# Kernel tuning notes

Hardware: AMD Instinct MI355X
Metric: run time of the kernel (lower is better)

## Reference

```python
import jax, jax.numpy as jnp
import numpy as np

P = 8          # patch_size
HEADS = 4      # patch_size // 2
DIM = 256      # nf*P*P // 16
DH = DIM // HEADS


def setup_inputs() -> dict:
    key = jax.random.key(0)
    ks = jax.random.split(key, 8)
    B, N, C, H, W = 8, 1, 64, 256, 256
    Np = (H // P) * (W // P)           # 1024
    patch_dim = C * P * P              # 4096
    s = 0.02
    return {
        "x": jax.random.normal(ks[0], (B, N, C, H, W), jnp.float32),
        "W_embed": jax.random.normal(ks[1], (DIM, patch_dim), jnp.float32) * s,
        "b_embed": jnp.zeros((DIM,), jnp.float32),
        "pos": jax.random.normal(ks[2], (1, Np, DIM), jnp.float32),
        "Wq": jax.random.normal(ks[3], (DIM, DIM), jnp.float32) * s,
        "Wk": jax.random.normal(ks[4], (Np, Np), jnp.float32) * s,
        "Wv": jax.random.normal(ks[5], (DIM, DIM), jnp.float32) * s,
        "Wout": jax.random.normal(ks[6], (patch_dim, DIM), jnp.float32) * s,
        "b_out": jnp.zeros((patch_dim,), jnp.float32),
    }


def reference(x, W_embed, b_embed, pos, Wq, Wk, Wv, Wout, b_out):
    B, N, C, H, W = x.shape
    Hp, Wp = H // P, W // P
    Np = Hp * Wp
    patch_dim = C * P * P
    BN = B * N

    # unfold (non-overlapping patches), column order = (C, kh, kw)
    xb = x.reshape(BN, C, Hp, P, Wp, P)
    patches = xb.transpose(0, 2, 4, 1, 3, 5).reshape(BN, Np, patch_dim)

    # linear_embed + positional embedding
    emb = jnp.einsum('bnp,dp->bnd', patches, W_embed) + b_embed + pos  # (BN, Np, DIM)

    # q: linear, split heads, mean over head-dim (AvgPool1d(dh) on length dh)
    q = jnp.einsum('bnd,ed->bne', emb, Wq)
    q = q.reshape(BN, Np, HEADS, DH).transpose(0, 2, 1, 3)  # (BN, H, Np, DH)
    q = q.mean(axis=-1)                                      # (BN, H, Np)

    # k = sigmoid(linear_k(q)); diag_embed(k) @ v == k[..., None] * v
    k = jax.nn.sigmoid(jnp.einsum('bhn,mn->bhm', q, Wk))     # (BN, H, Np)

    v = jnp.einsum('bnd,ed->bne', emb, Wv)
    v = v.reshape(BN, Np, HEADS, DH).transpose(0, 2, 1, 3)   # (BN, H, Np, DH)

    out = k[..., None] * v                                   # (BN, H, Np, DH)
    out = out.transpose(0, 2, 1, 3).reshape(BN, Np, DIM)

    out = jnp.einsum('bnd,pd->bnp', out, Wout) + b_out       # (BN, Np, patch_dim)

    # fold back to image
    out = out.reshape(BN, Hp, Wp, C, P, P).transpose(0, 3, 1, 4, 2, 5)
    out = out.reshape(B, N, C, H, W)
    return out
```

## Files before the change

### kernel.cpp

```cpp
#include <hip/hip_runtime.h>

typedef __attribute__((ext_vector_type(8))) short short8;
typedef __attribute__((ext_vector_type(4))) float f32x4;

#define LDA 72
#define KST 260

__device__ __forceinline__ unsigned short f2bf(float f) {
  unsigned int u = __builtin_bit_cast(unsigned int, f);
  u += 0x7fffu + ((u >> 16) & 1u);
  return (unsigned short)(u >> 16);
}
__device__ __forceinline__ float bf2f(unsigned short us) {
  return __builtin_bit_cast(float, (unsigned int)us << 16);
}

__device__ __forceinline__ void cvt_block(const float* __restrict__ src,
                                          unsigned short* __restrict__ dst, int b) {
  int i = b * 256 + threadIdx.x;
  float4 f = ((const float4*)src)[i];
  unsigned int lo = (unsigned int)f2bf(f.x) | ((unsigned int)f2bf(f.y) << 16);
  unsigned int hi = (unsigned int)f2bf(f.z) | ((unsigned int)f2bf(f.w) << 16);
  uint2 u; u.x = lo; u.y = hi;
  ((uint2*)dst)[i] = u;
}

__global__ __launch_bounds__(256) void prep_kernel(
    const float* __restrict__ W_embed, const float* __restrict__ Wout,
    const float* __restrict__ Wv, const float* __restrict__ Wq,
    unsigned short* __restrict__ Wb, unsigned short* __restrict__ Wob,
    unsigned short* __restrict__ Wvb, float* __restrict__ WqR) {
  int b = blockIdx.x;
  if (b < 1024) { cvt_block(W_embed, Wb, b); return; }
  if (b < 2048) { cvt_block(Wout, Wob, b - 1024); return; }
  if (b < 2112) { cvt_block(Wv, Wvb, b - 2048); return; }
  int idx = (b - 2112) * 256 + threadIdx.x;
  int h = idx >> 8, e = idx & 255;
  float s = 0.f;
  for (int j = 0; j < 64; ++j) s += Wq[(size_t)(h * 64 + j) * 256 + e];
  WqR[idx] = s * (1.f / 64.f);
}

__global__ __launch_bounds__(256) void gemm1_embed(
    const float* __restrict__ x, const unsigned short* __restrict__ Wb,
    float* __restrict__ part) {
  __shared__ __align__(16) unsigned short As[64 * LDA];
  __shared__ __align__(16) unsigned short Bs[128 * LDA];
  const int nt = blockIdx.x, mt = blockIdx.y, sk = blockIdx.z;
  const int m0 = mt * 64, n0 = nt * 128;
  const int t = threadIdx.x;
  const int wave = t >> 6, lane = t & 63;
  const int wm = wave >> 1, wn = wave & 1;
  const int lr = lane & 15, lq = lane >> 4;
  f32x4 acc[2][4];
#pragma unroll
  for (int i = 0; i < 2; i++)
#pragma unroll
    for (int j = 0; j < 4; j++) acc[i][j] = f32x4{0.f, 0.f, 0.f, 0.f};

  for (int kt = sk * 16; kt < sk * 16 + 16; ++kt) {
    const int k0 = kt * 64;
#pragma unroll
    for (int rr = 0; rr < 2; ++rr) {
      int r = t + rr * 256;
      int m = r >> 3, krun = r & 7;
      int gm = m0 + m;
      int bn = gm >> 10, nn = gm & 1023;
      int ph = nn >> 5, pw = nn & 31;
      int k = k0 + krun * 8;
      int c = k >> 6, kh = (k >> 3) & 7;
      const float* src = x + ((size_t)((bn << 6) + c) << 16) +
                         (size_t)((ph << 3) + kh) * 256 + (pw << 3);
      float4 f0 = *(const float4*)src;
      float4 f1 = *(const float4*)(src + 4);
      short8 v;
      v[0] = (short)f2bf(f0.x); v[1] = (short)f2bf(f0.y);
      v[2] = (short)f2bf(f0.z); v[3] = (short)f2bf(f0.w);
      v[4] = (short)f2bf(f1.x); v[5] = (short)f2bf(f1.y);
      v[6] = (short)f2bf(f1.z); v[7] = (short)f2bf(f1.w);
      *(short8*)&As[m * LDA + krun * 8] = v;
    }
#pragma unroll
    for (int rr = 0; rr < 4; ++rr) {
      int r = t + rr * 256;
      int n = r >> 3, krun = r & 7;
      *(short8*)&Bs[n * LDA + krun * 8] =
          *(const short8*)(Wb + (size_t)(n0 + n) * 4096 + k0 + krun * 8);
    }
    __syncthreads();
#pragma unroll
    for (int kc = 0; kc < 2; ++kc) {
      short8 a0 = *(const short8*)&As[(wm * 32 + lr) * LDA + kc * 32 + lq * 8];
      short8 a1 = *(const short8*)&As[(wm * 32 + 16 + lr) * LDA + kc * 32 + lq * 8];
#pragma unroll
      for (int ni = 0; ni < 4; ++ni) {
        short8 b = *(const short8*)&Bs[(wn * 64 + ni * 16 + lr) * LDA + kc * 32 + lq * 8];
        acc[0][ni] = __builtin_amdgcn_mfma_f32_16x16x32_bf16(a0, b, acc[0][ni], 0, 0, 0);
        acc[1][ni] = __builtin_amdgcn_mfma_f32_16x16x32_bf16(a1, b, acc[1][ni], 0, 0, 0);
      }
    }
    __syncthreads();
  }
  float* pdst = part + (size_t)sk * 2097152;
#pragma unroll
  for (int mi = 0; mi < 2; ++mi)
#pragma unroll
    for (int ni = 0; ni < 4; ++ni) {
      int col = n0 + wn * 64 + ni * 16 + lr;
      int rbase = m0 + wm * 32 + mi * 16 + lq * 4;
#pragma unroll
      for (int r2 = 0; r2 < 4; ++r2)
        pdst[(size_t)(rbase + r2) * 256 + col] = acc[mi][ni][r2];
    }
}

__global__ __launch_bounds__(256) void finq_kernel(
    const float* __restrict__ part, const float* __restrict__ b_embed,
    const float* __restrict__ pos, const float* __restrict__ WqR,
    unsigned short* __restrict__ emb_bf, float* __restrict__ q) {
  __shared__ float wq[1024];
  const int t = threadIdx.x;
  for (int i = t; i < 1024; i += 256) wq[i] = WqR[i];
  __syncthreads();
  const int row_l = t >> 3, seg = t & 7;
  const int row = blockIdx.x * 32 + row_l;
  const int bn = row >> 10, n = row & 1023;
  const float4* p4 = (const float4*)part;
  const float4* b4 = (const float4*)b_embed;
  const float4* pos4 = (const float4*)pos;
  const float4* wq4 = (const float4*)wq;
  const int idx0 = row * 64 + seg * 8;

  float4 e[8];
#pragma unroll
  for (int j = 0; j < 8; ++j) {
    float4 v = p4[idx0 + j];
    float4 v1 = p4[524288 + idx0 + j];
    float4 v2 = p4[1048576 + idx0 + j];
    float4 v3 = p4[1572864 + idx0 + j];
    float4 bb = b4[seg * 8 + j];
    float4 pp = pos4[(size_t)n * 64 + seg * 8 + j];
    e[j].x = v.x + v1.x + v2.x + v3.x + bb.x + pp.x;
    e[j].y = v.y + v1.y + v2.y + v3.y + bb.y + pp.y;
    e[j].z = v.z + v1.z + v2.z + v3.z + bb.z + pp.z;
    e[j].w = v.w + v1.w + v2.w + v3.w + bb.w + pp.w;
  }
  unsigned int ub[16];
#pragma unroll
  for (int j = 0; j < 8; ++j) {
    ub[2 * j]     = (unsigned int)f2bf(e[j].x) | ((unsigned int)f2bf(e[j].y) << 16);
    ub[2 * j + 1] = (unsigned int)f2bf(e[j].z) | ((unsigned int)f2bf(e[j].w) << 16);
  }
  uint4* dst = (uint4*)(emb_bf + (size_t)row * 256 + seg * 32);
#pragma unroll
  for (int j = 0; j < 4; ++j)
    dst[j] = make_uint4(ub[4 * j], ub[4 * j + 1], ub[4 * j + 2], ub[4 * j + 3]);
  float s[4] = {0.f, 0.f, 0.f, 0.f};
#pragma unroll
  for (int h = 0; h < 4; ++h)
#pragma unroll
    for (int j = 0; j < 8; ++j) {
      float4 w = wq4[h * 64 + seg * 8 + j];
      s[h] += e[j].x * w.x + e[j].y * w.y + e[j].z * w.z + e[j].w * w.w;
    }
#pragma unroll
  for (int h = 0; h < 4; ++h) {
    s[h] += __shfl_xor(s[h], 1);
    s[h] += __shfl_xor(s[h], 2);
    s[h] += __shfl_xor(s[h], 4);
  }
  if (seg == 0) {
#pragma unroll
    for (int h = 0; h < 4; ++h)
      q[(size_t)(bn * 4 + h) * 1024 + n] = s[h];
  }
}

__global__ __launch_bounds__(256) void k_kernel(const float* __restrict__ q,
                                                const float* __restrict__ Wk,
                                                float* __restrict__ kk) {
  __shared__ float wk_s[8 * KST];
  __shared__ float q_s[32 * KST];
  const int m0 = blockIdx.x * 8;
  const int t = threadIdx.x;
  const int m = t & 7, bh = t >> 3;
  const float4* wkg = (const float4*)Wk;
  const float4* qg = (const float4*)q;
  float acc = 0.f;
  for (int kt = 0; kt < 4; ++kt) {
    const int k0 = kt * 256;
#pragma unroll
    for (int i = 0; i < 2; ++i) {
      int idx = t + i * 256;
      int r = idx >> 6, c4 = idx & 63;
      *(float4*)&wk_s[r * KST + c4 * 4] = wkg[((size_t)(m0 + r) * 1024 + k0) / 4 + c4];
    }
#pragma unroll
    for (int i = 0; i < 8; ++i) {
      int idx = t + i * 256;
      int r = idx >> 6, c4 = idx & 63;
      *(float4*)&q_s[r * KST + c4 * 4] = qg[((size_t)r * 1024 + k0) / 4 + c4];
    }
    __syncthreads();
#pragma unroll 8
    for (int k4 = 0; k4 < 64; ++k4) {
      float4 a = *(const float4*)&wk_s[m * KST + k4 * 4];
      float4 b = *(const float4*)&q_s[bh * KST + k4 * 4];
      acc += a.x * b.x + a.y * b.y + a.z * b.z + a.w * b.w;
    }
    __syncthreads();
  }
  kk[(size_t)bh * 1024 + m0 + m] = 1.f / (1.f + __expf(-acc));
}

__global__ __launch_bounds__(256) void vgemm_kernel(
    const unsigned short* __restrict__ Abf, const unsigned short* __restrict__ Wvb,
    const float* __restrict__ kk, unsigned short* __restrict__ ov) {
  __shared__ __align__(16) unsigned short As[32 * LDA];
  __shared__ __align__(16) unsigned short Bs[64 * LDA];
  const int nt = blockIdx.x, mt = blockIdx.y;
  const int m0 = mt * 32, n0 = nt * 64;
  const int t = threadIdx.x;
  const int wave = t >> 6, lane = t & 63;
  const int wr = wave >> 1, wc = wave & 1;
  const int lr = lane & 15, lq = lane >> 4;
  f32x4 acc[2];
  acc[0] = f32x4{0.f, 0.f, 0.f, 0.f};
  acc[1] = f32x4{0.f, 0.f, 0.f, 0.f};

  for (int kt = 0; kt < 4; ++kt) {
    const int k0 = kt * 64;
    {
      int m = t >> 3, krun = t & 7;
      *(short8*)&As[m * LDA + krun * 8] =
          *(const short8*)(Abf + (size_t)(m0 + m) * 256 + k0 + krun * 8);
    }
#pragma unroll
    for (int rr = 0; rr < 2; ++rr) {
      int r = t + rr * 256;
      int n = r >> 3, krun = r & 7;
      *(short8*)&Bs[n * LDA + krun * 8] =
          *(const short8*)(Wvb + (size_t)(n0 + n) * 256 + k0 + krun * 8);
    }
    __syncthreads();
#pragma unroll
    for (int kc = 0; kc < 2; ++kc) {
      short8 a = *(const short8*)&As[(wr * 16 + lr) * LDA + kc * 32 + lq * 8];
#pragma unroll
      for (int ni = 0; ni < 2; ++ni) {
        short8 b = *(const short8*)&Bs[(wc * 32 + ni * 16 + lr) * LDA + kc * 32 + lq * 8];
        acc[ni] = __builtin_amdgcn_mfma_f32_16x16x32_bf16(a, b, acc[ni], 0, 0, 0);
      }
    }
    __syncthreads();
  }
#pragma unroll
  for (int ni = 0; ni < 2; ++ni) {
    int col = n0 + wc * 32 + ni * 16 + lr;
    int h = col >> 6;
    int rbase = m0 + wr * 16 + lq * 4;
#pragma unroll
    for (int r2 = 0; r2 < 4; ++r2) {
      int row = rbase + r2;
      int bn = row >> 10, n = row & 1023;
      float g = kk[(size_t)(bn * 4 + h) * 1024 + n];
      ov[(size_t)row * 256 + col] = f2bf(acc[ni][r2] * g);
    }
  }
}

#define CST 132
__global__ __launch_bounds__(256) void gemm2_out(
    const unsigned short* __restrict__ Abf, const unsigned short* __restrict__ Wob,
    const float* __restrict__ b_out, float* __restrict__ out) {
  __shared__ __align__(16) float smem[64 * CST];
  unsigned short* As = (unsigned short*)smem;
  unsigned short* Bs = As + 64 * LDA;
  const int nt = blockIdx.x, mt = blockIdx.y;
  const int m0 = mt * 64, n0 = nt * 128;
  const int t = threadIdx.x;
  const int wave = t >> 6, lane = t & 63;
  const int wm = wave >> 1, wn = wave & 1;
  const int lr = lane & 15, lq = lane >> 4;
  f32x4 acc[2][4];
#pragma unroll
  for (int i = 0; i < 2; i++)
#pragma unroll
    for (int j = 0; j < 4; j++) acc[i][j] = f32x4{0.f, 0.f, 0.f, 0.f};

  for (int kt = 0; kt < 4; ++kt) {
    const int k0 = kt * 64;
#pragma unroll
    for (int rr = 0; rr < 2; ++rr) {
      int r = t + rr * 256;
      int m = r >> 3, krun = r & 7;
      *(short8*)&As[m * LDA + krun * 8] =
          *(const short8*)(Abf + (size_t)(m0 + m) * 256 + k0 + krun * 8);
    }
#pragma unroll
    for (int rr = 0; rr < 4; ++rr) {
      int r = t + rr * 256;
      int n = r >> 3, krun = r & 7;
      *(short8*)&Bs[n * LDA + krun * 8] =
          *(const short8*)(Wob + (size_t)(n0 + n) * 256 + k0 + krun * 8);
    }
    __syncthreads();
#pragma unroll
    for (int kc = 0; kc < 2; ++kc) {
      short8 a0 = *(const short8*)&As[(wm * 32 + lr) * LDA + kc * 32 + lq * 8];
      short8 a1 = *(const short8*)&As[(wm * 32 + 16 + lr) * LDA + kc * 32 + lq * 8];
#pragma unroll
      for (int ni = 0; ni < 4; ++ni) {
        short8 b = *(const short8*)&Bs[(wn * 64 + ni * 16 + lr) * LDA + kc * 32 + lq * 8];
        acc[0][ni] = __builtin_amdgcn_mfma_f32_16x16x32_bf16(a0, b, acc[0][ni], 0, 0, 0);
        acc[1][ni] = __builtin_amdgcn_mfma_f32_16x16x32_bf16(a1, b, acc[1][ni], 0, 0, 0);
      }
    }
    __syncthreads();
  }
#pragma unroll
  for (int mi = 0; mi < 2; ++mi)
#pragma unroll
    for (int ni = 0; ni < 4; ++ni) {
      int pl = wn * 64 + ni * 16 + lr;
      int mb = wm * 32 + mi * 16 + lq * 4;
#pragma unroll
      for (int r2 = 0; r2 < 4; ++r2)
        smem[(mb + r2) * CST + pl] = acc[mi][ni][r2];
    }
  __syncthreads();
  const int bn = m0 >> 10;
  const int ph0 = (m0 & 1023) >> 5;
  const int c0 = n0 >> 6;
#pragma unroll
  for (int i = 0; i < 8; ++i) {
    int idx4 = t + i * 256;
    int kw4 = idx4 & 1;
    int pw = (idx4 >> 1) & 31;
    int kh = (idx4 >> 6) & 7;
    int c2 = (idx4 >> 9) & 1;
    int ph = (idx4 >> 10) & 1;
    int m_local = ph * 32 + pw;
    int p_local = c2 * 64 + kh * 8 + kw4 * 4;
    float4 v = *(const float4*)&smem[m_local * CST + p_local];
    float4 bo = *(const float4*)(b_out + n0 + p_local);
    v.x += bo.x; v.y += bo.y; v.z += bo.z; v.w += bo.w;
    size_t addr = ((size_t)((bn << 6) + c0 + c2) << 16) +
                  (size_t)(((ph0 + ph) << 3) + kh) * 256 + (pw << 3) + kw4 * 4;
    *(float4*)(out + addr) = v;
  }
}

extern "C" void kernel_launch(void* const* d_in, const int* in_sizes, int n_in,
                              void* d_out, int out_size, void* d_ws, size_t ws_size,
                              hipStream_t stream) {
  const float* x       = (const float*)d_in[0];
  const float* W_embed = (const float*)d_in[1];
  const float* b_embed = (const float*)d_in[2];
  const float* pos     = (const float*)d_in[3];
  const float* Wq      = (const float*)d_in[4];
  const float* Wk      = (const float*)d_in[5];
  const float* Wv      = (const float*)d_in[6];
  const float* Wout    = (const float*)d_in[7];
  const float* b_out   = (const float*)d_in[8];
  float* out = (float*)d_out;

  char* ws = (char*)d_ws;
  const size_t MB = 1024 * 1024;
  float* part            = (float*)(ws);
  unsigned short* ov     = (unsigned short*)(ws);
  unsigned short* emb_bf = (unsigned short*)(ws + 32 * MB);
  unsigned short* Wb     = (unsigned short*)(ws + 36 * MB);
  unsigned short* Wob    = (unsigned short*)(ws + 38 * MB);
  unsigned short* Wvb    = (unsigned short*)(ws + 40 * MB);
  float* q               = (float*)(ws + 40 * MB + 131072);
  float* kk              = (float*)(ws + 40 * MB + 262144);
  float* WqR             = (float*)(ws + 40 * MB + 393216);

  prep_kernel<<<2116, 256, 0, stream>>>(W_embed, Wout, Wv, Wq, Wb, Wob, Wvb, WqR);
  gemm1_embed<<<dim3(2, 128, 4), 256, 0, stream>>>(x, Wb, part);
  finq_kernel<<<256, 256, 0, stream>>>(part, b_embed, pos, WqR, emb_bf, q);
  k_kernel<<<128, 256, 0, stream>>>(q, Wk, kk);
  vgemm_kernel<<<dim3(4, 256), 256, 0, stream>>>(emb_bf, Wvb, kk, ov);
  gemm2_out<<<dim3(32, 128), 256, 0, stream>>>(ov, Wob, b_out, out);
}
```

Baseline: 357.1 us.

## Double-buffer gemm1 shared tiles with register prefetch and coalesced patch loads

The embedding GEMM now uses 512-thread blocks with 128x128 tiles and double-buffered LDS. The next k-tile is prefetched into registers while MFMAs run on the current buffer, which leaves one barrier per iteration instead of two. The A-tile loads are reorganised so a warp reads contiguous image rows of a patch row, giving more coalesced global loads. The trade-off is more LDS per block and higher register pressure, which may limit occupancy.

```diff
diff --git a/kernel.cpp b/kernel.cpp
--- a/kernel.cpp
+++ b/kernel.cpp
@@ -41,66 +41,114 @@
   WqR[idx] = s * (1.f / 64.f);
 }
 
-__global__ __launch_bounds__(256) void gemm1_embed(
+__global__ __launch_bounds__(512, 4) void gemm1_embed(
     const float* __restrict__ x, const unsigned short* __restrict__ Wb,
     float* __restrict__ part) {
-  __shared__ __align__(16) unsigned short As[64 * LDA];
-  __shared__ __align__(16) unsigned short Bs[128 * LDA];
+  __shared__ __align__(16) unsigned short sm[2][2][128 * LDA];
   const int nt = blockIdx.x, mt = blockIdx.y, sk = blockIdx.z;
-  const int m0 = mt * 64, n0 = nt * 128;
+  const int m0 = mt * 128, n0 = nt * 128;
   const int t = threadIdx.x;
   const int wave = t >> 6, lane = t & 63;
   const int wm = wave >> 1, wn = wave & 1;
   const int lr = lane & 15, lq = lane >> 4;
+
+  const int bn = m0 >> 10;
+  const int ph0 = (m0 & 1023) >> 5;
+
+  const int uA0 = t >> 5, colA = t & 31;
+  const int uA1 = uA0 + 16;
+  const float* xA = x + ((size_t)(bn << 6) << 16);
+  const float* pa0 = xA + (size_t)(((ph0 + (uA0 >> 3)) << 3) + (uA0 & 7)) * 256 + (colA << 3);
+  const float* pa1 = xA + (size_t)(((ph0 + (uA1 >> 3)) << 3) + (uA1 & 7)) * 256 + (colA << 3);
+  const int dA0 = (((uA0 >> 3) << 5) + colA) * LDA + ((uA0 & 7) << 3);
+  const int dA1 = (((uA1 >> 3) << 5) + colA) * LDA + ((uA1 & 7) << 3);
+
+  const int nB0 = t >> 3, kB = t & 7;
+  const int nB1 = nB0 + 64;
+  const unsigned short* pb0 = Wb + (size_t)(n0 + nB0) * 4096 + (kB << 3);
+  const unsigned short* pb1 = Wb + (size_t)(n0 + nB1) * 4096 + (kB << 3);
+  const int dB0 = nB0 * LDA + (kB << 3);
+  const int dB1 = nB1 * LDA + (kB << 3);
+
   f32x4 acc[2][4];
 #pragma unroll
   for (int i = 0; i < 2; i++)
 #pragma unroll
     for (int j = 0; j < 4; j++) acc[i][j] = f32x4{0.f, 0.f, 0.f, 0.f};
 
-  for (int kt = sk * 16; kt < sk * 16 + 16; ++kt) {
-    const int k0 = kt * 64;
-#pragma unroll
-    for (int rr = 0; rr < 2; ++rr) {
-      int r = t + rr * 256;
-      int m = r >> 3, krun = r & 7;
-      int gm = m0 + m;
-      int bn = gm >> 10, nn = gm & 1023;
-      int ph = nn >> 5, pw = nn & 31;
-      int k = k0 + krun * 8;
-      int c = k >> 6, kh = (k >> 3) & 7;
-      const float* src = x + ((size_t)((bn << 6) + c) << 16) +
-                         (size_t)((ph << 3) + kh) * 256 + (pw << 3);
-      float4 f0 = *(const float4*)src;
-      float4 f1 = *(const float4*)(src + 4);
-      short8 v;
-      v[0] = (short)f2bf(f0.x); v[1] = (short)f2bf(f0.y);
-      v[2] = (short)f2bf(f0.z); v[3] = (short)f2bf(f0.w);
-      v[4] = (short)f2bf(f1.x); v[5] = (short)f2bf(f1.y);
-      v[6] = (short)f2bf(f1.z); v[7] = (short)f2bf(f1.w);
-      *(short8*)&As[m * LDA + krun * 8] = v;
-    }
-#pragma unroll
-    for (int rr = 0; rr < 4; ++rr) {
-      int r = t + rr * 256;
-      int n = r >> 3, krun = r & 7;
-      *(short8*)&Bs[n * LDA + krun * 8] =
-          *(const short8*)(Wb + (size_t)(n0 + n) * 4096 + k0 + krun * 8);
-    }
-    __syncthreads();
+  float4 ra0, ra1, ra2, ra3;
+  short8 rb0, rb1;
+  const int kt0 = sk * 16;
+
+  {
+    const float* q0 = pa0 + (size_t)kt0 * 65536;
+    const float* q1 = pa1 + (size_t)kt0 * 65536;
+    ra0 = *(const float4*)q0; ra1 = *(const float4*)(q0 + 4);
+    ra2 = *(const float4*)q1; ra3 = *(const float4*)(q1 + 4);
+    rb0 = *(const short8*)(pb0 + kt0 * 64);
+    rb1 = *(const short8*)(pb1 + kt0 * 64);
+  }
+  {
+    short8 v0, v1;
+    v0[0] = (short)f2bf(ra0.x); v0[1] = (short)f2bf(ra0.y);
+    v0[2] = (short)f2bf(ra0.z); v0[3] = (short)f2bf(ra0.w);
+    v0[4] = (short)f2bf(ra1.x); v0[5] = (short)f2bf(ra1.y);
+    v0[6] = (short)f2bf(ra1.z); v0[7] = (short)f2bf(ra1.w);
+    v1[0] = (short)f2bf(ra2.x); v1[1] = (short)f2bf(ra2.y);
+    v1[2] = (short)f2bf(ra2.z); v1[3] = (short)f2bf(ra2.w);
+    v1[4] = (short)f2bf(ra3.x); v1[5] = (short)f2bf(ra3.y);
+    v1[6] = (short)f2bf(ra3.z); v1[7] = (short)f2bf(ra3.w);
+    *(short8*)&sm[0][0][dA0] = v0;
+    *(short8*)&sm[0][0][dA1] = v1;
+    *(short8*)&sm[0][1][dB0] = rb0;
+    *(short8*)&sm[0][1][dB1] = rb1;
+  }
+  __syncthreads();
+
+#pragma unroll 2
+  for (int i = 0; i < 16; ++i) {
+    if (i < 15) {
+      const int kt = kt0 + i + 1;
+      const float* q0 = pa0 + (size_t)kt * 65536;
+      const float* q1 = pa1 + (size_t)kt * 65536;
+      ra0 = *(const float4*)q0; ra1 = *(const float4*)(q0 + 4);
+      ra2 = *(const float4*)q1; ra3 = *(const float4*)(q1 + 4);
+      rb0 = *(const short8*)(pb0 + kt * 64);
+      rb1 = *(const short8*)(pb1 + kt * 64);
+    }
+    const unsigned short* Ab = sm[i & 1][0];
+    const unsigned short* Bb = sm[i & 1][1];
 #pragma unroll
     for (int kc = 0; kc < 2; ++kc) {
-      short8 a0 = *(const short8*)&As[(wm * 32 + lr) * LDA + kc * 32 + lq * 8];
-      short8 a1 = *(const short8*)&As[(wm * 32 + 16 + lr) * LDA + kc * 32 + lq * 8];
+      short8 a0 = *(const short8*)&Ab[(wm * 32 + lr) * LDA + kc * 32 + lq * 8];
+      short8 a1 = *(const short8*)&Ab[(wm * 32 + 16 + lr) * LDA + kc * 32 + lq * 8];
 #pragma unroll
       for (int ni = 0; ni < 4; ++ni) {
-        short8 b = *(const short8*)&Bs[(wn * 64 + ni * 16 + lr) * LDA + kc * 32 + lq * 8];
+        short8 b = *(const short8*)&Bb[(wn * 64 + ni * 16 + lr) * LDA + kc * 32 + lq * 8];
         acc[0][ni] = __builtin_amdgcn_mfma_f32_16x16x32_bf16(a0, b, acc[0][ni], 0, 0, 0);
         acc[1][ni] = __builtin_amdgcn_mfma_f32_16x16x32_bf16(a1, b, acc[1][ni], 0, 0, 0);
       }
     }
-    __syncthreads();
-  }
+    if (i < 15) {
+      unsigned short* Aw = sm[(i + 1) & 1][0];
+      unsigned short* Bw = sm[(i + 1) & 1][1];
+      short8 v0, v1;
+      v0[0] = (short)f2bf(ra0.x); v0[1] = (short)f2bf(ra0.y);
+      v0[2] = (short)f2bf(ra0.z); v0[3] = (short)f2bf(ra0.w);
+      v0[4] = (short)f2bf(ra1.x); v0[5] = (short)f2bf(ra1.y);
+      v0[6] = (short)f2bf(ra1.z); v0[7] = (short)f2bf(ra1.w);
+      v1[0] = (short)f2bf(ra2.x); v1[1] = (short)f2bf(ra2.y);
+      v1[2] = (short)f2bf(ra2.z); v1[3] = (short)f2bf(ra2.w);
+      v1[4] = (short)f2bf(ra3.x); v1[5] = (short)f2bf(ra3.y);
+      v1[6] = (short)f2bf(ra3.z); v1[7] = (short)f2bf(ra3.w);
+      *(short8*)&Aw[dA0] = v0;
+      *(short8*)&Aw[dA1] = v1;
+      *(short8*)&Bw[dB0] = rb0;
+      *(short8*)&Bw[dB1] = rb1;
+      __syncthreads();
+    }
+  }
+
   float* pdst = part + (size_t)sk * 2097152;
 #pragma unroll
   for (int mi = 0; mi < 2; ++mi)
@@ -378,7 +426,7 @@
   float* WqR             = (float*)(ws + 40 * MB + 393216);
 
   prep_kernel<<<2116, 256, 0, stream>>>(W_embed, Wout, Wv, Wq, Wb, Wob, Wvb, WqR);
-  gemm1_embed<<<dim3(2, 128, 4), 256, 0, stream>>>(x, Wb, part);
+  gemm1_embed<<<dim3(2, 64, 4), 512, 0, stream>>>(x, Wb, part);
   finq_kernel<<<256, 256, 0, stream>>>(part, b_embed, pos, WqR, emb_bf, q);
   k_kernel<<<128, 256, 0, stream>>>(q, Wk, kk);
   vgemm_kernel<<<dim3(4, 256), 256, 0, stream>>>(emb_bf, Wvb, kk, ov);
```

New measurement: 331.8 us. 1.08x faster.

## Double-buffer GEMM tiles with register prefetch and enlarge embed/v tiles

Applied to the files above, without the earlier changes.

The embed GEMM now uses 512-thread blocks over 128-row tiles, with a patch-aware coalesced load mapping. Its K loop is a two-stage register prefetch into double-buffered shared memory, so global loads overlap the MFMA work. The output GEMM gets the same double-buffered prefetch pipeline. The V GEMM loads its whole K=256 slab into shared memory once, using 64-row tiles, which removes the per-step barriers. These changes raise shared memory and register use per block, which may reduce occupancy.

```diff
diff --git a/kernel.cpp b/kernel.cpp
--- a/kernel.cpp
+++ b/kernel.cpp
@@ -13,6 +13,32 @@
 }
 __device__ __forceinline__ float bf2f(unsigned short us) {
   return __builtin_bit_cast(float, (unsigned int)us << 16);
+}
+
+__device__ __forceinline__ short8 cvt8(float4 lo, float4 hi) {
+  short8 v;
+  v[0] = (short)f2bf(lo.x); v[1] = (short)f2bf(lo.y);
+  v[2] = (short)f2bf(lo.z); v[3] = (short)f2bf(lo.w);
+  v[4] = (short)f2bf(hi.x); v[5] = (short)f2bf(hi.y);
+  v[6] = (short)f2bf(hi.z); v[7] = (short)f2bf(hi.w);
+  return v;
+}
+
+__device__ __forceinline__ void mfma_tile(const unsigned short* __restrict__ Ab,
+                                          const unsigned short* __restrict__ Bb,
+                                          int wm, int wn, int lr, int lq,
+                                          f32x4 (&acc)[2][4]) {
+#pragma unroll
+  for (int kc = 0; kc < 2; ++kc) {
+    short8 a0 = *(const short8*)&Ab[(wm * 32 + lr) * LDA + kc * 32 + lq * 8];
+    short8 a1 = *(const short8*)&Ab[(wm * 32 + 16 + lr) * LDA + kc * 32 + lq * 8];
+#pragma unroll
+    for (int ni = 0; ni < 4; ++ni) {
+      short8 b = *(const short8*)&Bb[(wn * 64 + ni * 16 + lr) * LDA + kc * 32 + lq * 8];
+      acc[0][ni] = __builtin_amdgcn_mfma_f32_16x16x32_bf16(a0, b, acc[0][ni], 0, 0, 0);
+      acc[1][ni] = __builtin_amdgcn_mfma_f32_16x16x32_bf16(a1, b, acc[1][ni], 0, 0, 0);
+    }
+  }
 }
 
 __device__ __forceinline__ void cvt_block(const float* __restrict__ src,
@@ -41,66 +67,90 @@
   WqR[idx] = s * (1.f / 64.f);
 }
 
-__global__ __launch_bounds__(256) void gemm1_embed(
+struct StageG1 { float4 a0, a1, a2, a3; short8 b0, b1; };
+
+__device__ __forceinline__ void g1_load(StageG1& s, const float* q0, const float* q1,
+                                        const unsigned short* b0, const unsigned short* b1) {
+  s.a0 = *(const float4*)q0; s.a1 = *(const float4*)(q0 + 4);
+  s.a2 = *(const float4*)q1; s.a3 = *(const float4*)(q1 + 4);
+  s.b0 = *(const short8*)b0; s.b1 = *(const short8*)b1;
+}
+
+__device__ __forceinline__ void g1_write(unsigned short* Aw, unsigned short* Bw,
+                                         int dA0, int dA1, int dB0, int dB1,
+                                         const StageG1& s) {
+  *(short8*)&Aw[dA0] = cvt8(s.a0, s.a1);
+  *(short8*)&Aw[dA1] = cvt8(s.a2, s.a3);
+  *(short8*)&Bw[dB0] = s.b0;
+  *(short8*)&Bw[dB1] = s.b1;
+}
+
+__global__ __launch_bounds__(512, 4) void gemm1_embed(
     const float* __restrict__ x, const unsigned short* __restrict__ Wb,
     float* __restrict__ part) {
-  __shared__ __align__(16) unsigned short As[64 * LDA];
-  __shared__ __align__(16) unsigned short Bs[128 * LDA];
+  __shared__ __align__(16) unsigned short sm[2][2][128 * LDA];
   const int nt = blockIdx.x, mt = blockIdx.y, sk = blockIdx.z;
-  const int m0 = mt * 64, n0 = nt * 128;
+  const int m0 = mt * 128, n0 = nt * 128;
   const int t = threadIdx.x;
   const int wave = t >> 6, lane = t & 63;
   const int wm = wave >> 1, wn = wave & 1;
   const int lr = lane & 15, lq = lane >> 4;
+
+  const int bn = m0 >> 10;
+  const int ph0 = (m0 & 1023) >> 5;
+
+  const int uA0 = t >> 5, colA = t & 31;
+  const int uA1 = uA0 + 16;
+  const float* xA = x + ((size_t)(bn << 6) << 16);
+  const float* pa0 = xA + (size_t)(((ph0 + (uA0 >> 3)) << 3) + (uA0 & 7)) * 256 + (colA << 3);
+  const float* pa1 = xA + (size_t)(((ph0 + (uA1 >> 3)) << 3) + (uA1 & 7)) * 256 + (colA << 3);
+  const int dA0 = (((uA0 >> 3) << 5) + colA) * LDA + ((uA0 & 7) << 3);
+  const int dA1 = (((uA1 >> 3) << 5) + colA) * LDA + ((uA1 & 7) << 3);
+
+  const int nB0 = t >> 3, kB = t & 7;
+  const int nB1 = nB0 + 64;
+  const unsigned short* pb0 = Wb + (size_t)(n0 + nB0) * 4096 + (kB << 3);
+  const unsigned short* pb1 = Wb + (size_t)(n0 + nB1) * 4096 + (kB << 3);
+  const int dB0 = nB0 * LDA + (kB << 3);
+  const int dB1 = nB1 * LDA + (kB << 3);
+
   f32x4 acc[2][4];
 #pragma unroll
   for (int i = 0; i < 2; i++)
 #pragma unroll
     for (int j = 0; j < 4; j++) acc[i][j] = f32x4{0.f, 0.f, 0.f, 0.f};
 
-  for (int kt = sk * 16; kt < sk * 16 + 16; ++kt) {
-    const int k0 = kt * 64;
-#pragma unroll
-    for (int rr = 0; rr < 2; ++rr) {
-      int r = t + rr * 256;
-      int m = r >> 3, krun = r & 7;
-      int gm = m0 + m;
-      int bn = gm >> 10, nn = gm & 1023;
-      int ph = nn >> 5, pw = nn & 31;
-      int k = k0 + krun * 8;
-      int c = k >> 6, kh = (k >> 3) & 7;
-      const float* src = x + ((size_t)((bn << 6) + c) << 16) +
-                         (size_t)((ph << 3) + kh) * 256 + (pw << 3);
-      float4 f0 = *(const float4*)src;
-      float4 f1 = *(const float4*)(src + 4);
-      short8 v;
-      v[0] = (short)f2bf(f0.x); v[1] = (short)f2bf(f0.y);
-      v[2] = (short)f2bf(f0.z); v[3] = (short)f2bf(f0.w);
-      v[4] = (short)f2bf(f1.x); v[5] = (short)f2bf(f1.y);
-      v[6] = (short)f2bf(f1.z); v[7] = (short)f2bf(f1.w);
-      *(short8*)&As[m * LDA + krun * 8] = v;
-    }
-#pragma unroll
-    for (int rr = 0; rr < 4; ++rr) {
-      int r = t + rr * 256;
-      int n = r >> 3, krun = r & 7;
-      *(short8*)&Bs[n * LDA + krun * 8] =
-          *(const short8*)(Wb + (size_t)(n0 + n) * 4096 + k0 + krun * 8);
-    }
+  unsigned short* A0 = &sm[0][0][0]; unsigned short* B0 = &sm[0][1][0];
+  unsigned short* A1 = &sm[1][0][0]; unsigned short* B1 = &sm[1][1][0];
+
+  StageG1 st0, st1;
+  const int kt0 = sk * 16;
+  g1_load(st0, pa0 + (size_t)kt0 * 65536, pa1 + (size_t)kt0 * 65536,
+          pb0 + (size_t)kt0 * 64, pb1 + (size_t)kt0 * 64);
+  g1_load(st1, pa0 + (size_t)(kt0 + 1) * 65536, pa1 + (size_t)(kt0 + 1) * 65536,
+          pb0 + (size_t)(kt0 + 1) * 64, pb1 + (size_t)(kt0 + 1) * 64);
+  g1_write(A0, B0, dA0, dA1, dB0, dB1, st0);
+  __syncthreads();
+
+#pragma unroll 1
+  for (int p = 0; p < 7; ++p) {
+    const int kb = kt0 + 2 * p;
+    g1_load(st0, pa0 + (size_t)(kb + 2) * 65536, pa1 + (size_t)(kb + 2) * 65536,
+            pb0 + (size_t)(kb + 2) * 64, pb1 + (size_t)(kb + 2) * 64);
+    mfma_tile(A0, B0, wm, wn, lr, lq, acc);
+    g1_write(A1, B1, dA0, dA1, dB0, dB1, st1);
     __syncthreads();
-#pragma unroll
-    for (int kc = 0; kc < 2; ++kc) {
-      short8 a0 = *(const short8*)&As[(wm * 32 + lr) * LDA + kc * 32 + lq * 8];
-      short8 a1 = *(const short8*)&As[(wm * 32 + 16 + lr) * LDA + kc * 32 + lq * 8];
-#pragma unroll
-      for (int ni = 0; ni < 4; ++ni) {
-        short8 b = *(const short8*)&Bs[(wn * 64 + ni * 16 + lr) * LDA + kc * 32 + lq * 8];
-        acc[0][ni] = __builtin_amdgcn_mfma_f32_16x16x32_bf16(a0, b, acc[0][ni], 0, 0, 0);
-        acc[1][ni] = __builtin_amdgcn_mfma_f32_16x16x32_bf16(a1, b, acc[1][ni], 0, 0, 0);
-      }
-    }
+    g1_load(st1, pa0 + (size_t)(kb + 3) * 65536, pa1 + (size_t)(kb + 3) * 65536,
+            pb0 + (size_t)(kb + 3) * 64, pb1 + (size_t)(kb + 3) * 64);
+    mfma_tile(A1, B1, wm, wn, lr, lq, acc);
+    g1_write(A0, B0, dA0, dA1, dB0, dB1, st0);
     __syncthreads();
   }
+  mfma_tile(A0, B0, wm, wn, lr, lq, acc);
+  g1_write(A1, B1, dA0, dA1, dB0, dB1, st1);
+  __syncthreads();
+  mfma_tile(A1, B1, wm, wn, lr, lq, acc);
+
   float* pdst = part + (size_t)sk * 2097152;
 #pragma unroll
   for (int mi = 0; mi < 2; ++mi)
@@ -213,111 +263,129 @@
   kk[(size_t)bh * 1024 + m0 + m] = 1.f / (1.f + __expf(-acc));
 }
 
+#define VST 264
 __global__ __launch_bounds__(256) void vgemm_kernel(
     const unsigned short* __restrict__ Abf, const unsigned short* __restrict__ Wvb,
     const float* __restrict__ kk, unsigned short* __restrict__ ov) {
-  __shared__ __align__(16) unsigned short As[32 * LDA];
-  __shared__ __align__(16) unsigned short Bs[64 * LDA];
+  __shared__ __align__(16) unsigned short Vs[128 * VST];
   const int nt = blockIdx.x, mt = blockIdx.y;
-  const int m0 = mt * 32, n0 = nt * 64;
+  const int m0 = mt * 64, n0 = nt * 64;
   const int t = threadIdx.x;
   const int wave = t >> 6, lane = t & 63;
   const int wr = wave >> 1, wc = wave & 1;
   const int lr = lane & 15, lq = lane >> 4;
-  f32x4 acc[2];
-  acc[0] = f32x4{0.f, 0.f, 0.f, 0.f};
-  acc[1] = f32x4{0.f, 0.f, 0.f, 0.f};
-
-  for (int kt = 0; kt < 4; ++kt) {
-    const int k0 = kt * 64;
-    {
-      int m = t >> 3, krun = t & 7;
-      *(short8*)&As[m * LDA + krun * 8] =
-          *(const short8*)(Abf + (size_t)(m0 + m) * 256 + k0 + krun * 8);
-    }
-#pragma unroll
-    for (int rr = 0; rr < 2; ++rr) {
-      int r = t + rr * 256;
-      int n = r >> 3, krun = r & 7;
-      *(short8*)&Bs[n * LDA + krun * 8] =
-          *(const short8*)(Wvb + (size_t)(n0 + n) * 256 + k0 + krun * 8);
-    }
-    __syncthreads();
-#pragma unroll
-    for (int kc = 0; kc < 2; ++kc) {
-      short8 a = *(const short8*)&As[(wr * 16 + lr) * LDA + kc * 32 + lq * 8];
-#pragma unroll
-      for (int ni = 0; ni < 2; ++ni) {
-        short8 b = *(const short8*)&Bs[(wc * 32 + ni * 16 + lr) * LDA + kc * 32 + lq * 8];
-        acc[ni] = __builtin_amdgcn_mfma_f32_16x16x32_bf16(a, b, acc[ni], 0, 0, 0);
+
+  const int row0 = t >> 5, kb = t & 31;
+#pragma unroll
+  for (int i = 0; i < 8; ++i)
+    *(short8*)&Vs[(row0 + i * 8) * VST + kb * 8] =
+        *(const short8*)(Abf + (size_t)(m0 + row0 + i * 8) * 256 + kb * 8);
+#pragma unroll
+  for (int i = 0; i < 8; ++i)
+    *(short8*)&Vs[(64 + row0 + i * 8) * VST + kb * 8] =
+        *(const short8*)(Wvb + (size_t)(n0 + row0 + i * 8) * 256 + kb * 8);
+  __syncthreads();
+
+  f32x4 acc[2][2];
+#pragma unroll
+  for (int i = 0; i < 2; ++i)
+#pragma unroll
+    for (int j = 0; j < 2; ++j) acc[i][j] = f32x4{0.f, 0.f, 0.f, 0.f};
+
+#pragma unroll
+  for (int kc = 0; kc < 8; ++kc) {
+    short8 a0 = *(const short8*)&Vs[(wr * 32 + lr) * VST + kc * 32 + lq * 8];
+    short8 a1 = *(const short8*)&Vs[(wr * 32 + 16 + lr) * VST + kc * 32 + lq * 8];
+    short8 b0 = *(const short8*)&Vs[(64 + wc * 32 + lr) * VST + kc * 32 + lq * 8];
+    short8 b1 = *(const short8*)&Vs[(64 + wc * 32 + 16 + lr) * VST + kc * 32 + lq * 8];
+    acc[0][0] = __builtin_amdgcn_mfma_f32_16x16x32_bf16(a0, b0, acc[0][0], 0, 0, 0);
+    acc[0][1] = __builtin_amdgcn_mfma_f32_16x16x32_bf16(a0, b1, acc[0][1], 0, 0, 0);
+    acc[1][0] = __builtin_amdgcn_mfma_f32_16x16x32_bf16(a1, b0, acc[1][0], 0, 0, 0);
+    acc[1][1] = __builtin_amdgcn_mfma_f32_16x16x32_bf16(a1, b1, acc[1][1], 0, 0, 0);
+  }
+
+#pragma unroll
+  for (int mi = 0; mi < 2; ++mi)
+#pragma unroll
+    for (int ni = 0; ni < 2; ++ni) {
+      int col = n0 + wc * 32 + ni * 16 + lr;
+      int h = col >> 6;
+      int rbase = m0 + wr * 32 + mi * 16 + lq * 4;
+#pragma unroll
+      for (int r2 = 0; r2 < 4; ++r2) {
+        int row = rbase + r2;
+        int bn = row >> 10, n = row & 1023;
+        float g = kk[(size_t)(bn * 4 + h) * 1024 + n];
+        ov[(size_t)row * 256 + col] = f2bf(acc[mi][ni][r2] * g);
       }
     }
-    __syncthreads();
-  }
-#pragma unroll
-  for (int ni = 0; ni < 2; ++ni) {
-    int col = n0 + wc * 32 + ni * 16 + lr;
-    int h = col >> 6;
-    int rbase = m0 + wr * 16 + lq * 4;
-#pragma unroll
-    for (int r2 = 0; r2 < 4; ++r2) {
-      int row = rbase + r2;
-      int bn = row >> 10, n = row & 1023;
-      float g = kk[(size_t)(bn * 4 + h) * 1024 + n];
-      ov[(size_t)row * 256 + col] = f2bf(acc[ni][r2] * g);
-    }
-  }
 }
 
 #define CST 132
-__global__ __launch_bounds__(256) void gemm2_out(
+struct StageG2 { short8 a[2]; short8 b[4]; };
+
+__device__ __forceinline__ void g2_load(StageG2& s, const unsigned short* pA,
+                                        const unsigned short* pB, int k0) {
+#pragma unroll
+  for (int i = 0; i < 2; ++i)
+    s.a[i] = *(const short8*)(pA + (size_t)i * 32 * 256 + k0);
+#pragma unroll
+  for (int i = 0; i < 4; ++i)
+    s.b[i] = *(const short8*)(pB + (size_t)i * 32 * 256 + k0);
+}
+__device__ __forceinline__ void g2_write(unsigned short* Ab, unsigned short* Bb,
+                                         int dA, int dB, const StageG2& s) {
+#pragma unroll
+  for (int i = 0; i < 2; ++i) *(short8*)&Ab[dA + i * 32 * LDA] = s.a[i];
+#pragma unroll
+  for (int i = 0; i < 4; ++i) *(short8*)&Bb[dB + i * 32 * LDA] = s.b[i];
+}
+
+__global__ __launch_bounds__(256, 2) void gemm2_out(
     const unsigned short* __restrict__ Abf, const unsigned short* __restrict__ Wob,
     const float* __restrict__ b_out, float* __restrict__ out) {
-  __shared__ __align__(16) float smem[64 * CST];
-  unsigned short* As = (unsigned short*)smem;
-  unsigned short* Bs = As + 64 * LDA;
+  __shared__ __align__(16) unsigned short smbuf[2][192 * LDA];
+  float* csm = (float*)&smbuf[0][0];
   const int nt = blockIdx.x, mt = blockIdx.y;
   const int m0 = mt * 64, n0 = nt * 128;
   const int t = threadIdx.x;
   const int wave = t >> 6, lane = t & 63;
   const int wm = wave >> 1, wn = wave & 1;
   const int lr = lane & 15, lq = lane >> 4;
+
+  unsigned short* A0 = &smbuf[0][0]; unsigned short* B0 = &smbuf[0][64 * LDA];
+  unsigned short* A1 = &smbuf[1][0]; unsigned short* B1 = &smbuf[1][64 * LDA];
+
+  const unsigned short* pA = Abf + (size_t)(m0 + (t >> 3)) * 256 + (t & 7) * 8;
+  const unsigned short* pB = Wob + (size_t)(n0 + (t >> 3)) * 256 + (t & 7) * 8;
+  const int dA = (t >> 3) * LDA + (t & 7) * 8;
+  const int dB = dA;
+
   f32x4 acc[2][4];
 #pragma unroll
   for (int i = 0; i < 2; i++)
 #pragma unroll
     for (int j = 0; j < 4; j++) acc[i][j] = f32x4{0.f, 0.f, 0.f, 0.f};
 
-  for (int kt = 0; kt < 4; ++kt) {
-    const int k0 = kt * 64;
-#pragma unroll
-    for (int rr = 0; rr < 2; ++rr) {
-      int r = t + rr * 256;
-      int m = r >> 3, krun = r & 7;
-      *(short8*)&As[m * LDA + krun * 8] =
-          *(const short8*)(Abf + (size_t)(m0 + m) * 256 + k0 + krun * 8);
-    }
-#pragma unroll
-    for (int rr = 0; rr < 4; ++rr) {
-      int r = t + rr * 256;
-      int n = r >> 3, krun = r & 7;
-      *(short8*)&Bs[n * LDA + krun * 8] =
-          *(const short8*)(Wob + (size_t)(n0 + n) * 256 + k0 + krun * 8);
-    }
-    __syncthreads();
-#pragma unroll
-    for (int kc = 0; kc < 2; ++kc) {
-      short8 a0 = *(const short8*)&As[(wm * 32 + lr) * LDA + kc * 32 + lq * 8];
-      short8 a1 = *(const short8*)&As[(wm * 32 + 16 + lr) * LDA + kc * 32 + lq * 8];
-#pragma unroll
-      for (int ni = 0; ni < 4; ++ni) {
-        short8 b = *(const short8*)&Bs[(wn * 64 + ni * 16 + lr) * LDA + kc * 32 + lq * 8];
-        acc[0][ni] = __builtin_amdgcn_mfma_f32_16x16x32_bf16(a0, b, acc[0][ni], 0, 0, 0);
-        acc[1][ni] = __builtin_amdgcn_mfma_f32_16x16x32_bf16(a1, b, acc[1][ni], 0, 0, 0);
-      }
-    }
-    __syncthreads();
-  }
+  StageG2 st0, st1;
+  g2_load(st0, pA, pB, 0);
+  g2_load(st1, pA, pB, 64);
+  g2_write(A0, B0, dA, dB, st0);
+  __syncthreads();
+  g2_load(st0, pA, pB, 128);
+  mfma_tile(A0, B0, wm, wn, lr, lq, acc);
+  g2_write(A1, B1, dA, dB, st1);
+  __syncthreads();
+  g2_load(st1, pA, pB, 192);
+  mfma_tile(A1, B1, wm, wn, lr, lq, acc);
+  g2_write(A0, B0, dA, dB, st0);
+  __syncthreads();
+  mfma_tile(A0, B0, wm, wn, lr, lq, acc);
+  g2_write(A1, B1, dA, dB, st1);
+  __syncthreads();
+  mfma_tile(A1, B1, wm, wn, lr, lq, acc);
+  __syncthreads();
+
 #pragma unroll
   for (int mi = 0; mi < 2; ++mi)
 #pragma unroll
@@ -326,7 +394,7 @@
       int mb = wm * 32 + mi * 16 + lq * 4;
 #pragma unroll
       for (int r2 = 0; r2 < 4; ++r2)
-        smem[(mb + r2) * CST + pl] = acc[mi][ni][r2];
+        csm[(mb + r2) * CST + pl] = acc[mi][ni][r2];
     }
   __syncthreads();
   const int bn = m0 >> 10;
@@ -342,7 +410,7 @@
     int ph = (idx4 >> 10) & 1;
     int m_local = ph * 32 + pw;
     int p_local = c2 * 64 + kh * 8 + kw4 * 4;
-    float4 v = *(const float4*)&smem[m_local * CST + p_local];
+    float4 v = *(const float4*)&csm[m_local * CST + p_local];
     float4 bo = *(const float4*)(b_out + n0 + p_local);
     v.x += bo.x; v.y += bo.y; v.z += bo.z; v.w += bo.w;
     size_t addr = ((size_t)((bn << 6) + c0 + c2) << 16) +
@@ -378,9 +446,9 @@
   float* WqR             = (float*)(ws + 40 * MB + 393216);
 
   prep_kernel<<<2116, 256, 0, stream>>>(W_embed, Wout, Wv, Wq, Wb, Wob, Wvb, WqR);
-  gemm1_embed<<<dim3(2, 128, 4), 256, 0, stream>>>(x, Wb, part);
+  gemm1_embed<<<dim3(2, 64, 4), 512, 0, stream>>>(x, Wb, part);
   finq_kernel<<<256, 256, 0, stream>>>(part, b_embed, pos, WqR, emb_bf, q);
   k_kernel<<<128, 256, 0, stream>>>(q, Wk, kk);
-  vgemm_kernel<<<dim3(4, 256), 256, 0, stream>>>(emb_bf, Wvb, kk, ov);
+  vgemm_kernel<<<dim3(4, 128), 256, 0, stream>>>(emb_bf, Wvb, kk, ov);
   gemm2_out<<<dim3(32, 128), 256, 0, stream>>>(ov, Wob, b_out, out);
 }
```

Result: faster. 334.0 us (-6.5%).
